# Performance work log

Hardware: AMD Instinct MI355X
Metric: run time of the kernel (lower is better)

The kernel has to match this reference:

```python
import jax, jax.numpy as jnp
import numpy as np

B, T, C = 2, 2048, 2048
NH, NKV, D = 16, 4, 128
N_REP = NH // NKV
THETA = 10000.0


def setup_inputs() -> dict:
    key = jax.random.key(0)
    ks = jax.random.split(key, 5)
    s = 0.02
    return {
        "x": jax.random.normal(ks[0], (B, T, C), dtype=jnp.float32),
        "Wq": jax.random.normal(ks[1], (C, C), dtype=jnp.float32) * s,
        "Wk": jax.random.normal(ks[2], (NKV * D, C), dtype=jnp.float32) * s,
        "Wv": jax.random.normal(ks[3], (NKV * D, C), dtype=jnp.float32) * s,
        "Wo": jax.random.normal(ks[4], (C, C), dtype=jnp.float32) * s,
    }


def _rope(t):
    # t: (B, H, T, D); rotate pairs (even, odd) by angle pos * theta_i
    inv_freq = 1.0 / (THETA ** (jnp.arange(0, D, 2, dtype=jnp.float32) / D))  # (D/2,)
    ang = jnp.arange(T, dtype=jnp.float32)[:, None] * inv_freq[None, :]       # (T, D/2)
    cos, sin = jnp.cos(ang), jnp.sin(ang)
    te, to = t[..., 0::2], t[..., 1::2]
    re = te * cos - to * sin
    ro = te * sin + to * cos
    return jnp.stack([re, ro], axis=-1).reshape(t.shape).astype(t.dtype)


def reference(x, Wq, Wk, Wv, Wo):
    # Projections (Linear: y = x @ W.T)
    q = (x @ Wq.T).reshape(B, T, NH, D).transpose(0, 2, 1, 3)    # (B,NH,T,D)
    k = (x @ Wk.T).reshape(B, T, NKV, D).transpose(0, 2, 1, 3)   # (B,NKV,T,D)
    v = (x @ Wv.T).reshape(B, T, NKV, D).transpose(0, 2, 1, 3)
    q = _rope(q)
    k = _rope(k)
    # GQA: group query heads per kv head instead of materializing repeated K/V
    qg = q.reshape(B, NKV, N_REP, T, D)                          # (B,G,R,T,D)
    scale = 1.0 / jnp.sqrt(jnp.float32(D))
    scores = jnp.einsum("bgrtd,bgsd->bgrts", qg, k) * scale      # (B,G,R,T,T)
    causal = jnp.tril(jnp.ones((T, T), dtype=bool))
    scores = jnp.where(causal, scores, jnp.finfo(scores.dtype).min)
    attn = jax.nn.softmax(scores, axis=-1)
    out = jnp.einsum("bgrts,bgsd->bgrtd", attn, v)               # (B,G,R,T,D)
    out = out.reshape(B, NH, T, D).transpose(0, 2, 1, 3).reshape(B, T, C)
    return out @ Wo.T
```

## Files before the change

kernel.cpp:

```cpp
#include <hip/hip_runtime.h>
#include <hip/hip_bf16.h>
#include <stdint.h>

#define B_   2
#define T_   2048
#define C_   2048
#define NH_  16
#define NKV_ 4
#define D_   128
#define NREP_ 4

typedef __attribute__((ext_vector_type(8))) short bf16x8;
typedef __attribute__((ext_vector_type(4))) float f32x4;

__device__ inline short f2bs(float f) {
    __hip_bfloat16 h = __float2bfloat16(f);
    return *reinterpret_cast<short*>(&h);
}
__device__ inline float bs2f(unsigned short s) {
    __hip_bfloat16 h = *reinterpret_cast<__hip_bfloat16*>(&s);
    return __bfloat162float(h);
}

__device__ inline void gl_lds16(const __hip_bfloat16* g, __hip_bfloat16* l) {
    __builtin_amdgcn_global_load_lds(
        (const __attribute__((address_space(1))) unsigned int*)g,
        (__attribute__((address_space(3))) unsigned int*)l,
        16, 0, 0);
}

__global__ void cvt_f32_bf16(const float* __restrict__ src,
                             __hip_bfloat16* __restrict__ dst, int n) {
    int i = (blockIdx.x * blockDim.x + threadIdx.x) * 4;
    if (i >= n) return;
    float4 v = *reinterpret_cast<const float4*>(src + i);
    short4 o;
    o.x = f2bs(v.x); o.y = f2bs(v.y); o.z = f2bs(v.z); o.w = f2bs(v.w);
    *reinterpret_cast<short4*>(dst + i) = o;
}

__device__ inline void storeC(float* p, float v) { *p = v; }
__device__ inline void storeC(__hip_bfloat16* p, float v) { *p = __float2bfloat16(v); }

template <typename OutT>
__global__ __launch_bounds__(256) void gemm_bt(const __hip_bfloat16* __restrict__ A,
                                               const __hip_bfloat16* __restrict__ Bm,
                                               OutT* __restrict__ Cm,
                                               int M, int N, int K) {
    __shared__ __hip_bfloat16 As[128 * 32];
    __shared__ __hip_bfloat16 Bs[128 * 32];
    const int tid  = threadIdx.x;
    const int lane = tid & 63;
    const int wv   = tid >> 6;
    const int m0 = blockIdx.y * 128, n0 = blockIdx.x * 128;
    const int wm = (wv >> 1) * 64, wn = (wv & 1) * 64;
    const int q16 = lane >> 4, r16 = lane & 15;

    f32x4 acc[4][4] = {};

    const int lrow = tid >> 2;
    const int lcol = (tid & 3) * 8;
    const __hip_bfloat16* aG = A  + (size_t)(m0 + lrow) * K + lcol;
    const __hip_bfloat16* bG = Bm + (size_t)(n0 + lrow) * K + lcol;
    __hip_bfloat16* aL = As + tid * 8;
    __hip_bfloat16* bL = Bs + tid * 8;

    for (int k0 = 0; k0 < K; k0 += 32) {
        __syncthreads();
        gl_lds16(aG + k0,          aL);
        gl_lds16(aG + 64 * K + k0, aL + 2048);
        gl_lds16(bG + k0,          bL);
        gl_lds16(bG + 64 * K + k0, bL + 2048);
        __syncthreads();
        bf16x8 af[4], bfr[4];
#pragma unroll
        for (int i = 0; i < 4; i++)
            af[i] = *reinterpret_cast<const bf16x8*>(As + (wm + i * 16 + r16) * 32 + q16 * 8);
#pragma unroll
        for (int j = 0; j < 4; j++)
            bfr[j] = *reinterpret_cast<const bf16x8*>(Bs + (wn + j * 16 + r16) * 32 + q16 * 8);
#pragma unroll
        for (int i = 0; i < 4; i++)
#pragma unroll
            for (int j = 0; j < 4; j++)
                acc[i][j] = __builtin_amdgcn_mfma_f32_16x16x32_bf16(af[i], bfr[j], acc[i][j], 0, 0, 0);
    }

#pragma unroll
    for (int i = 0; i < 4; i++)
#pragma unroll
        for (int j = 0; j < 4; j++)
#pragma unroll
            for (int r = 0; r < 4; r++) {
                int row = m0 + wm + i * 16 + q16 * 4 + r;
                int col = n0 + wn + j * 16 + r16;
                storeC(&Cm[(size_t)row * N + col], acc[i][j][r]);
            }
}

__global__ void rope_scatter(const __hip_bfloat16* __restrict__ y,
                             __hip_bfloat16* __restrict__ qo,
                             __hip_bfloat16* __restrict__ ko,
                             __hip_bfloat16* __restrict__ vT) {
    int idx = blockIdx.x * blockDim.x + threadIdx.x;
    if (idx >= (B_ * T_) * 1536) return;
    int m = idx / 1536, pc = idx % 1536;
    int b = m / T_, t = m % T_;
    int n = pc * 2;
    ushort2 uv = *reinterpret_cast<const ushort2*>(y + (size_t)m * 3072 + n);
    float e = bs2f(uv.x), od = bs2f(uv.y);

    if (n < 2560) {
        int nn = (n < 2048) ? n : (n - 2048);
        int dloc = nn & 127;
        int p = dloc >> 1;
        float inv = __expf(-(float)p * (9.210340371976184f / 64.0f));
        float ang = (float)t * inv;
        float c = cosf(ang), s = sinf(ang);
        float re = e * c - od * s;
        float ro = e * s + od * c;
        ushort2 w;
        w.x = (unsigned short)f2bs(re);
        w.y = (unsigned short)f2bs(ro);
        if (n < 2048) {
            int h = n >> 7;
            *reinterpret_cast<ushort2*>(qo + ((size_t)(b * NH_ + h) * T_ + t) * D_ + dloc) = w;
        } else {
            int h = nn >> 7;
            *reinterpret_cast<ushort2*>(ko + ((size_t)(b * NKV_ + h) * T_ + t) * D_ + dloc) = w;
        }
    } else {
        int nn = n - 2560;
        int h = nn >> 7, d = nn & 127;
        __hip_bfloat16* base = vT + (size_t)(b * NKV_ + h) * D_ * T_;
        base[(size_t)d * T_ + t]       = __float2bfloat16(e);
        base[(size_t)(d + 1) * T_ + t] = __float2bfloat16(od);
    }
}

__device__ inline bf16x8 pf_gather(const ushort4& w0, const ushort4& w1,
                                   int q16, int r16) {
    int2 a0 = *reinterpret_cast<const int2*>(&w0);
    int2 a1 = *reinterpret_cast<const int2*>(&w1);
    int srcLo = ((q16 & 1) << 5) + r16;
    int srcHi = srcLo + 16;
    int lo0x = __shfl(a0.x, srcLo), lo0y = __shfl(a0.y, srcLo);
    int lo1x = __shfl(a1.x, srcLo), lo1y = __shfl(a1.y, srcLo);
    int hi0x = __shfl(a0.x, srcHi), hi0y = __shfl(a0.y, srcHi);
    int hi1x = __shfl(a1.x, srcHi), hi1y = __shfl(a1.y, srcHi);
    bool lw = (q16 < 2);
    int4 pk;
    pk.x = lw ? lo0x : lo1x;
    pk.y = lw ? lo0y : lo1y;
    pk.z = lw ? hi0x : hi1x;
    pk.w = lw ? hi0y : hi1y;
    return *reinterpret_cast<bf16x8*>(&pk);
}

__global__ __launch_bounds__(256, 3) void attn_kernel(const __hip_bfloat16* __restrict__ Q,
                                                      const __hip_bfloat16* __restrict__ Kt,
                                                      const __hip_bfloat16* __restrict__ Vt,
                                                      __hip_bfloat16* __restrict__ Op0,
                                                      __hip_bfloat16* __restrict__ Op1,
                                                      float* __restrict__ LiP) {
    __shared__ __hip_bfloat16 Ks[2][4096];
    __shared__ __hip_bfloat16 Vs[2][4096];

    const int lane = threadIdx.x & 63, wv = threadIdx.x >> 6;
    const int bg = blockIdx.y;
    const int xr = 127 - (int)blockIdx.x;
    const int tb = xr >> 1, half = xr & 1;
    const int b = bg >> 2, g = bg & 3;
    const int h = g * 4 + wv;
    const int t0 = tb * 32;
    const int q16 = lane >> 4, r16 = lane & 15;

    const int n = tb + 1;

    const __hip_bfloat16* qh = Q + ((size_t)((b * NH_ + h) * T_) + t0) * D_;
    const __hip_bfloat16* kh = Kt + (size_t)(b * NKV_ + g) * T_ * D_;
    const __hip_bfloat16* vh = Vt + (size_t)(b * NKV_ + g) * D_ * T_;

    bf16x8 bqA[4], bqB[4];
#pragma unroll
    for (int kk = 0; kk < 4; kk++) {
        bqA[kk] = *reinterpret_cast<const bf16x8*>(qh + (size_t)r16 * D_ + kk * 32 + q16 * 8);
        bqB[kk] = *reinterpret_cast<const bf16x8*>(qh + (size_t)(16 + r16) * D_ + kk * 32 + q16 * 8);
    }

    float liA = 0.f, liB = 0.f;
    f32x4 oA[8], oB[8];
#pragma unroll
    for (int d = 0; d < 8; d++) {
        oA[d] = (f32x4){0.f, 0.f, 0.f, 0.f};
        oB[d] = (f32x4){0.f, 0.f, 0.f, 0.f};
    }

    const float SCL2 = 0.088388347648318447f * 1.4426950408889634f;
    const int tqA = t0 + r16;
    const int tqB = t0 + 16 + r16;

    const __hip_bfloat16* gK = kh + (size_t)((wv & 1) * 16 + r16) * D_ + q16 * 8;
    const __hip_bfloat16* gV = vh + (size_t)(((wv - 2) * 4) * 16 + r16) * T_ + q16 * 8;

#define STAGE(bufi, s0_)                                                        \
    do {                                                                        \
        if (wv < 2) {                                                           \
            const __hip_bfloat16* gp = gK + (size_t)(s0_) * D_;                 \
            __hip_bfloat16* lp = &Ks[bufi][(wv * 4) * 512] + lane * 8;          \
            gl_lds16(gp,      lp);                                              \
            gl_lds16(gp + 32, lp + 512);                                        \
            gl_lds16(gp + 64, lp + 1024);                                       \
            gl_lds16(gp + 96, lp + 1536);                                       \
        } else {                                                                \
            const __hip_bfloat16* gp = gV + (s0_);                              \
            __hip_bfloat16* lp = &Vs[bufi][((wv - 2) * 4) * 512] + lane * 8;    \
            gl_lds16(gp,                      lp);                              \
            gl_lds16(gp + (size_t)16 * T_,    lp + 512);                        \
            gl_lds16(gp + (size_t)32 * T_,    lp + 1024);                       \
            gl_lds16(gp + (size_t)48 * T_,    lp + 1536);                       \
        }                                                                       \
    } while (0)

    if (half < n) STAGE(0, half * 32);

    int j = 0;
    for (int it = half; it < n; it += 2, j++) {
        const int s0 = it * 32;
        const int cur = j & 1;
        __syncthreads();
        if (it + 2 < n) STAGE(cur ^ 1, (it + 2) * 32);

        f32x4 sc0A = (f32x4){0.f, 0.f, 0.f, 0.f};
        f32x4 sc1A = (f32x4){0.f, 0.f, 0.f, 0.f};
        f32x4 sc0B = (f32x4){0.f, 0.f, 0.f, 0.f};
        f32x4 sc1B = (f32x4){0.f, 0.f, 0.f, 0.f};
        {
            bf16x8 ak[4];
#pragma unroll
            for (int kk = 0; kk < 4; kk++)
                ak[kk] = *reinterpret_cast<const bf16x8*>(&Ks[cur][kk * 512] + lane * 8);
#pragma unroll
            for (int kk = 0; kk < 4; kk++) {
                sc0A = __builtin_amdgcn_mfma_f32_16x16x32_bf16(ak[kk], bqA[kk], sc0A, 0, 0, 0);
                sc0B = __builtin_amdgcn_mfma_f32_16x16x32_bf16(ak[kk], bqB[kk], sc0B, 0, 0, 0);
            }
#pragma unroll
            for (int kk = 0; kk < 4; kk++)
                ak[kk] = *reinterpret_cast<const bf16x8*>(&Ks[cur][(4 + kk) * 512] + lane * 8);
#pragma unroll
            for (int kk = 0; kk < 4; kk++) {
                sc1A = __builtin_amdgcn_mfma_f32_16x16x32_bf16(ak[kk], bqA[kk], sc1A, 0, 0, 0);
                sc1B = __builtin_amdgcn_mfma_f32_16x16x32_bf16(ak[kk], bqB[kk], sc1B, 0, 0, 0);
            }
        }

        ushort4 w0A, w1A, w0B, w1B;
        float psA = 0.f, psB = 0.f;
#pragma unroll
        for (int r = 0; r < 4; r++) {
            int s_a = s0 + q16 * 4 + r;
            float pa0 = (s_a <= tqA)      ? __builtin_amdgcn_exp2f(sc0A[r] * SCL2) : 0.f;
            float pa1 = (s_a + 16 <= tqA) ? __builtin_amdgcn_exp2f(sc1A[r] * SCL2) : 0.f;
            float pb0 = (s_a <= tqB)      ? __builtin_amdgcn_exp2f(sc0B[r] * SCL2) : 0.f;
            float pb1 = (s_a + 16 <= tqB) ? __builtin_amdgcn_exp2f(sc1B[r] * SCL2) : 0.f;
            psA += pa0 + pa1;
            psB += pb0 + pb1;
            ((unsigned short*)&w0A)[r] = (unsigned short)f2bs(pa0);
            ((unsigned short*)&w1A)[r] = (unsigned short)f2bs(pa1);
            ((unsigned short*)&w0B)[r] = (unsigned short)f2bs(pb0);
            ((unsigned short*)&w1B)[r] = (unsigned short)f2bs(pb1);
        }
        liA += psA;
        liB += psB;

        bf16x8 pfA = pf_gather(w0A, w1A, q16, r16);
        bf16x8 pfB = pf_gather(w0B, w1B, q16, r16);

#pragma unroll
        for (int d = 0; d < 8; d++) {
            bf16x8 bv = *reinterpret_cast<const bf16x8*>(&Vs[cur][d * 512] + lane * 8);
            oA[d] = __builtin_amdgcn_mfma_f32_16x16x32_bf16(pfA, bv, oA[d], 0, 0, 0);
            oB[d] = __builtin_amdgcn_mfma_f32_16x16x32_bf16(pfB, bv, oB[d], 0, 0, 0);
        }
    }

    liA += __shfl_xor(liA, 16);
    liA += __shfl_xor(liA, 32);
    liB += __shfl_xor(liB, 16);
    liB += __shfl_xor(liB, 32);

    const int tile = bg * 64 + tb;
    __hip_bfloat16* od = (half ? Op1 : Op0) + ((size_t)(tile * 4 + wv)) * 4096;
#pragma unroll
    for (int r = 0; r < 4; r++) {
        int qA = q16 * 4 + r;
#pragma unroll
        for (int d = 0; d < 8; d++) {
            od[qA * 128 + d * 16 + r16]        = __float2bfloat16(oA[d][r]);
            od[(qA + 16) * 128 + d * 16 + r16] = __float2bfloat16(oB[d][r]);
        }
    }
    float* lp = LiP + ((size_t)(tile * 2 + half)) * 128 + wv * 32;
    if (q16 == 0) lp[r16] = liA;
    if (q16 == 1) lp[16 + r16] = liB;
#undef STAGE
}

__global__ void attn_combine(const __hip_bfloat16* __restrict__ O0,
                             const __hip_bfloat16* __restrict__ O1,
                             const float* __restrict__ Li,
                             __hip_bfloat16* __restrict__ Ao) {
    int idx = blockIdx.x * blockDim.x + threadIdx.x;
    int dv   = idx & 15;
    int q    = (idx >> 4) & 31;
    int hw   = (idx >> 9) & 3;
    int tile = idx >> 11;
    int bg = tile >> 6, tb = tile & 63;
    int b = bg >> 2, g = bg & 3;

    size_t obase = ((size_t)(tile * 4 + hw)) * 4096 + q * 128 + dv * 8;
    bf16x8 v0 = *reinterpret_cast<const bf16x8*>(O0 + obase);
    bf16x8 v1 = *reinterpret_cast<const bf16x8*>(O1 + obase);
    float li = Li[(size_t)(tile * 2) * 128 + hw * 32 + q] +
               Li[(size_t)(tile * 2 + 1) * 128 + hw * 32 + q];
    float inv = 1.0f / li;

    int t = tb * 32 + q;
    int h = g * 4 + hw;
    bf16x8 ov;
#pragma unroll
    for (int j = 0; j < 8; j++) {
        float s = bs2f(((const unsigned short*)&v0)[j]) + bs2f(((const unsigned short*)&v1)[j]);
        ov[j] = f2bs(s * inv);
    }
    *reinterpret_cast<bf16x8*>(Ao + ((size_t)(b * T_ + t)) * C_ + h * D_ + dv * 8) = ov;
}

extern "C" void kernel_launch(void* const* d_in, const int* in_sizes, int n_in,
                              void* d_out, int out_size, void* d_ws, size_t ws_size,
                              hipStream_t stream) {
    const float* x  = (const float*)d_in[0];
    const float* Wq = (const float*)d_in[1];
    const float* Wk = (const float*)d_in[2];
    const float* Wv = (const float*)d_in[3];
    const float* Wo = (const float*)d_in[4];
    float* out = (float*)d_out;
    char* ws = (char*)d_ws;

    __hip_bfloat16* xb   = (__hip_bfloat16*)(ws + 0);
    __hip_bfloat16* wcat = (__hip_bfloat16*)(ws + 16777216);
    __hip_bfloat16* wob  = (__hip_bfloat16*)(ws + 29360128);
    __hip_bfloat16* yq   = (__hip_bfloat16*)(ws + 37748736);
    __hip_bfloat16* qatt = (__hip_bfloat16*)(ws + 62914560);
    __hip_bfloat16* katt = (__hip_bfloat16*)(ws + 79691776);
    __hip_bfloat16* vT   = (__hip_bfloat16*)(ws + 83886080);
    __hip_bfloat16* aout = (__hip_bfloat16*)(ws + 88080384);

    __hip_bfloat16* Op0 = (__hip_bfloat16*)(ws + 0);
    __hip_bfloat16* Op1 = (__hip_bfloat16*)(ws + 37748736);
    float*          LiP = (float*)(ws + 54525952);

    const int thr = 256;
    cvt_f32_bf16<<<(B_ * T_ * C_ / 4 + thr - 1) / thr, thr, 0, stream>>>(x, xb, B_ * T_ * C_);
    cvt_f32_bf16<<<(C_ * C_ / 4 + thr - 1) / thr, thr, 0, stream>>>(Wq, wcat, C_ * C_);
    cvt_f32_bf16<<<(512 * 2048 / 4 + thr - 1) / thr, thr, 0, stream>>>(Wk, wcat + C_ * C_, 512 * 2048);
    cvt_f32_bf16<<<(512 * 2048 / 4 + thr - 1) / thr, thr, 0, stream>>>(Wv, wcat + C_ * C_ + 512 * 2048, 512 * 2048);
    cvt_f32_bf16<<<(C_ * C_ / 4 + thr - 1) / thr, thr, 0, stream>>>(Wo, wob, C_ * C_);

    gemm_bt<__hip_bfloat16><<<dim3(24, 32), 256, 0, stream>>>(xb, wcat, yq, 4096, 3072, 2048);

    rope_scatter<<<(B_ * T_ * 1536 + thr - 1) / thr, thr, 0, stream>>>(yq, qatt, katt, vT);

    attn_kernel<<<dim3(128, 8), 256, 0, stream>>>(qatt, katt, vT, Op0, Op1, LiP);
    attn_combine<<<4096, 256, 0, stream>>>(Op0, Op1, LiP, aout);

    gemm_bt<float><<<dim3(16, 32), 256, 0, stream>>>(aout, wob, out, 4096, 2048, 2048);
}
```

Before: 348.8 us.

## Enlarge attention query tile, merge conversions, split V transpose kernel

Attention blocks now each handle 64 query rows per head as four 16-row subtiles. Each K/V tile staged in LDS is reused across twice as many queries, and fully masked subtiles skip their score MFMAs. The five f32-to-bf16 conversion launches become one kernel. The V transpose moves out of the RoPE kernel into its own kernel that writes 8-element vectors instead of scattered scalar stores. The larger tile raises register pressure (occupancy hint lowered from 3 to 2) and halves the grid, which risks worse load balance.

```diff
diff --git a/kernel.cpp b/kernel.cpp
--- a/kernel.cpp
+++ b/kernel.cpp
@@ -29,10 +29,20 @@
         16, 0, 0);
 }
 
-__global__ void cvt_f32_bf16(const float* __restrict__ src,
-                             __hip_bfloat16* __restrict__ dst, int n) {
-    int i = (blockIdx.x * blockDim.x + threadIdx.x) * 4;
-    if (i >= n) return;
+__global__ void cvt_all(const float* __restrict__ x,  const float* __restrict__ Wq,
+                        const float* __restrict__ Wk, const float* __restrict__ Wv,
+                        const float* __restrict__ Wo,
+                        __hip_bfloat16* __restrict__ xb,
+                        __hip_bfloat16* __restrict__ wcat,
+                        __hip_bfloat16* __restrict__ wob) {
+    int q = blockIdx.x * blockDim.x + threadIdx.x;
+    const float* src; __hip_bfloat16* dst; int off;
+    if (q < 2097152)      { src = x;  dst = xb;             off = q; }
+    else if (q < 3145728) { src = Wq; dst = wcat;           off = q - 2097152; }
+    else if (q < 3407872) { src = Wk; dst = wcat + 4194304; off = q - 3145728; }
+    else if (q < 3670016) { src = Wv; dst = wcat + 5242880; off = q - 3407872; }
+    else                  { src = Wo; dst = wob;            off = q - 3670016; }
+    int i = off * 4;
     float4 v = *reinterpret_cast<const float4*>(src + i);
     short4 o;
     o.x = f2bs(v.x); o.y = f2bs(v.y); o.z = f2bs(v.z); o.w = f2bs(v.w);
@@ -98,44 +108,58 @@
             }
 }
 
-__global__ void rope_scatter(const __hip_bfloat16* __restrict__ y,
-                             __hip_bfloat16* __restrict__ qo,
-                             __hip_bfloat16* __restrict__ ko,
-                             __hip_bfloat16* __restrict__ vT) {
+__global__ void rope_qk(const __hip_bfloat16* __restrict__ y,
+                        __hip_bfloat16* __restrict__ qo,
+                        __hip_bfloat16* __restrict__ ko) {
     int idx = blockIdx.x * blockDim.x + threadIdx.x;
-    if (idx >= (B_ * T_) * 1536) return;
-    int m = idx / 1536, pc = idx % 1536;
+    if (idx >= (B_ * T_) * 1280) return;
+    int m = idx / 1280, pc = idx % 1280;
     int b = m / T_, t = m % T_;
     int n = pc * 2;
     ushort2 uv = *reinterpret_cast<const ushort2*>(y + (size_t)m * 3072 + n);
     float e = bs2f(uv.x), od = bs2f(uv.y);
 
-    if (n < 2560) {
-        int nn = (n < 2048) ? n : (n - 2048);
-        int dloc = nn & 127;
-        int p = dloc >> 1;
-        float inv = __expf(-(float)p * (9.210340371976184f / 64.0f));
-        float ang = (float)t * inv;
-        float c = cosf(ang), s = sinf(ang);
-        float re = e * c - od * s;
-        float ro = e * s + od * c;
-        ushort2 w;
-        w.x = (unsigned short)f2bs(re);
-        w.y = (unsigned short)f2bs(ro);
-        if (n < 2048) {
-            int h = n >> 7;
-            *reinterpret_cast<ushort2*>(qo + ((size_t)(b * NH_ + h) * T_ + t) * D_ + dloc) = w;
-        } else {
-            int h = nn >> 7;
-            *reinterpret_cast<ushort2*>(ko + ((size_t)(b * NKV_ + h) * T_ + t) * D_ + dloc) = w;
-        }
+    int nn = (n < 2048) ? n : (n - 2048);
+    int dloc = nn & 127;
+    int p = dloc >> 1;
+    float inv = __expf(-(float)p * (9.210340371976184f / 64.0f));
+    float ang = (float)t * inv;
+    float c = cosf(ang), s = sinf(ang);
+    float re = e * c - od * s;
+    float ro = e * s + od * c;
+    ushort2 w;
+    w.x = (unsigned short)f2bs(re);
+    w.y = (unsigned short)f2bs(ro);
+    if (n < 2048) {
+        int h = n >> 7;
+        *reinterpret_cast<ushort2*>(qo + ((size_t)(b * NH_ + h) * T_ + t) * D_ + dloc) = w;
     } else {
-        int nn = n - 2560;
-        int h = nn >> 7, d = nn & 127;
-        __hip_bfloat16* base = vT + (size_t)(b * NKV_ + h) * D_ * T_;
-        base[(size_t)d * T_ + t]       = __float2bfloat16(e);
-        base[(size_t)(d + 1) * T_ + t] = __float2bfloat16(od);
-    }
+        int h = nn >> 7;
+        *reinterpret_cast<ushort2*>(ko + ((size_t)(b * NKV_ + h) * T_ + t) * D_ + dloc) = w;
+    }
+}
+
+__global__ void v_transpose(const __hip_bfloat16* __restrict__ y,
+                            __hip_bfloat16* __restrict__ vT) {
+    int idx = blockIdx.x * blockDim.x + threadIdx.x;
+    int tc = idx & 255;
+    int d  = (idx >> 8) & 127;
+    int gg = (idx >> 15) & 3;
+    int b  = idx >> 17;
+    int t0 = tc * 8;
+    const __hip_bfloat16* src = y + (size_t)(b * T_ + t0) * 3072 + 2560 + gg * 128 + d;
+    ushort4 w0, w1;
+    ((unsigned short*)&w0)[0] = *(const unsigned short*)(src);
+    ((unsigned short*)&w0)[1] = *(const unsigned short*)(src + 3072);
+    ((unsigned short*)&w0)[2] = *(const unsigned short*)(src + 2 * 3072);
+    ((unsigned short*)&w0)[3] = *(const unsigned short*)(src + 3 * 3072);
+    ((unsigned short*)&w1)[0] = *(const unsigned short*)(src + 4 * 3072);
+    ((unsigned short*)&w1)[1] = *(const unsigned short*)(src + 5 * 3072);
+    ((unsigned short*)&w1)[2] = *(const unsigned short*)(src + 6 * 3072);
+    ((unsigned short*)&w1)[3] = *(const unsigned short*)(src + 7 * 3072);
+    __hip_bfloat16* dst = vT + ((size_t)(b * NKV_ + gg) * D_ + d) * T_ + t0;
+    *reinterpret_cast<ushort4*>(dst)     = w0;
+    *reinterpret_cast<ushort4*>(dst + 4) = w1;
 }
 
 __device__ inline bf16x8 pf_gather(const ushort4& w0, const ushort4& w1,
@@ -157,7 +181,7 @@
     return *reinterpret_cast<bf16x8*>(&pk);
 }
 
-__global__ __launch_bounds__(256, 3) void attn_kernel(const __hip_bfloat16* __restrict__ Q,
+__global__ __launch_bounds__(256, 2) void attn_kernel(const __hip_bfloat16* __restrict__ Q,
                                                       const __hip_bfloat16* __restrict__ Kt,
                                                       const __hip_bfloat16* __restrict__ Vt,
                                                       __hip_bfloat16* __restrict__ Op0,
@@ -168,37 +192,35 @@
 
     const int lane = threadIdx.x & 63, wv = threadIdx.x >> 6;
     const int bg = blockIdx.y;
-    const int xr = 127 - (int)blockIdx.x;
+    const int xr = 63 - (int)blockIdx.x;
     const int tb = xr >> 1, half = xr & 1;
     const int b = bg >> 2, g = bg & 3;
     const int h = g * 4 + wv;
-    const int t0 = tb * 32;
+    const int t0 = tb * 64;
     const int q16 = lane >> 4, r16 = lane & 15;
 
-    const int n = tb + 1;
+    const int n = 2 * (tb + 1);
 
     const __hip_bfloat16* qh = Q + ((size_t)((b * NH_ + h) * T_) + t0) * D_;
     const __hip_bfloat16* kh = Kt + (size_t)(b * NKV_ + g) * T_ * D_;
     const __hip_bfloat16* vh = Vt + (size_t)(b * NKV_ + g) * D_ * T_;
 
-    bf16x8 bqA[4], bqB[4];
-#pragma unroll
-    for (int kk = 0; kk < 4; kk++) {
-        bqA[kk] = *reinterpret_cast<const bf16x8*>(qh + (size_t)r16 * D_ + kk * 32 + q16 * 8);
-        bqB[kk] = *reinterpret_cast<const bf16x8*>(qh + (size_t)(16 + r16) * D_ + kk * 32 + q16 * 8);
-    }
-
-    float liA = 0.f, liB = 0.f;
-    f32x4 oA[8], oB[8];
-#pragma unroll
-    for (int d = 0; d < 8; d++) {
-        oA[d] = (f32x4){0.f, 0.f, 0.f, 0.f};
-        oB[d] = (f32x4){0.f, 0.f, 0.f, 0.f};
-    }
+    bf16x8 bq[4][4];
+#pragma unroll
+    for (int tile = 0; tile < 4; tile++)
+#pragma unroll
+        for (int kk = 0; kk < 4; kk++)
+            bq[tile][kk] = *reinterpret_cast<const bf16x8*>(
+                qh + (size_t)(tile * 16 + r16) * D_ + kk * 32 + q16 * 8);
+
+    float li[4] = {0.f, 0.f, 0.f, 0.f};
+    f32x4 acc[4][8];
+#pragma unroll
+    for (int tile = 0; tile < 4; tile++)
+#pragma unroll
+        for (int d = 0; d < 8; d++) acc[tile][d] = (f32x4){0.f, 0.f, 0.f, 0.f};
 
     const float SCL2 = 0.088388347648318447f * 1.4426950408889634f;
-    const int tqA = t0 + r16;
-    const int tqB = t0 + 16 + r16;
 
     const __hip_bfloat16* gK = kh + (size_t)((wv & 1) * 16 + r16) * D_ + q16 * 8;
     const __hip_bfloat16* gV = vh + (size_t)(((wv - 2) * 4) * 16 + r16) * T_ + q16 * 8;
@@ -231,79 +253,74 @@
         __syncthreads();
         if (it + 2 < n) STAGE(cur ^ 1, (it + 2) * 32);
 
-        f32x4 sc0A = (f32x4){0.f, 0.f, 0.f, 0.f};
-        f32x4 sc1A = (f32x4){0.f, 0.f, 0.f, 0.f};
-        f32x4 sc0B = (f32x4){0.f, 0.f, 0.f, 0.f};
-        f32x4 sc1B = (f32x4){0.f, 0.f, 0.f, 0.f};
-        {
-            bf16x8 ak[4];
-#pragma unroll
-            for (int kk = 0; kk < 4; kk++)
-                ak[kk] = *reinterpret_cast<const bf16x8*>(&Ks[cur][kk * 512] + lane * 8);
-#pragma unroll
-            for (int kk = 0; kk < 4; kk++) {
-                sc0A = __builtin_amdgcn_mfma_f32_16x16x32_bf16(ak[kk], bqA[kk], sc0A, 0, 0, 0);
-                sc0B = __builtin_amdgcn_mfma_f32_16x16x32_bf16(ak[kk], bqB[kk], sc0B, 0, 0, 0);
-            }
-#pragma unroll
-            for (int kk = 0; kk < 4; kk++)
-                ak[kk] = *reinterpret_cast<const bf16x8*>(&Ks[cur][(4 + kk) * 512] + lane * 8);
-#pragma unroll
-            for (int kk = 0; kk < 4; kk++) {
-                sc1A = __builtin_amdgcn_mfma_f32_16x16x32_bf16(ak[kk], bqA[kk], sc1A, 0, 0, 0);
-                sc1B = __builtin_amdgcn_mfma_f32_16x16x32_bf16(ak[kk], bqB[kk], sc1B, 0, 0, 0);
+        bf16x8 akl[4], akh[4];
+#pragma unroll
+        for (int kk = 0; kk < 4; kk++) {
+            akl[kk] = *reinterpret_cast<const bf16x8*>(&Ks[cur][kk * 512] + lane * 8);
+            akh[kk] = *reinterpret_cast<const bf16x8*>(&Ks[cur][(4 + kk) * 512] + lane * 8);
+        }
+
+        bf16x8 pf[4];
+#pragma unroll
+        for (int tile = 0; tile < 4; tile++) {
+            if (s0 <= t0 + tile * 16 + 15) {
+                f32x4 sc0 = (f32x4){0.f, 0.f, 0.f, 0.f};
+                f32x4 sc1 = (f32x4){0.f, 0.f, 0.f, 0.f};
+#pragma unroll
+                for (int kk = 0; kk < 4; kk++) {
+                    sc0 = __builtin_amdgcn_mfma_f32_16x16x32_bf16(akl[kk], bq[tile][kk], sc0, 0, 0, 0);
+                    sc1 = __builtin_amdgcn_mfma_f32_16x16x32_bf16(akh[kk], bq[tile][kk], sc1, 0, 0, 0);
+                }
+                const int tq = t0 + tile * 16 + r16;
+                ushort4 w0, w1;
+                float ps = 0.f;
+#pragma unroll
+                for (int r = 0; r < 4; r++) {
+                    int s_a = s0 + q16 * 4 + r;
+                    float p0 = (s_a <= tq)      ? __builtin_amdgcn_exp2f(sc0[r] * SCL2) : 0.f;
+                    float p1 = (s_a + 16 <= tq) ? __builtin_amdgcn_exp2f(sc1[r] * SCL2) : 0.f;
+                    ps += p0 + p1;
+                    ((unsigned short*)&w0)[r] = (unsigned short)f2bs(p0);
+                    ((unsigned short*)&w1)[r] = (unsigned short)f2bs(p1);
+                }
+                li[tile] += ps;
+                pf[tile] = pf_gather(w0, w1, q16, r16);
+            } else {
+                int4 z = (int4){0, 0, 0, 0};
+                pf[tile] = *reinterpret_cast<bf16x8*>(&z);
             }
         }
 
-        ushort4 w0A, w1A, w0B, w1B;
-        float psA = 0.f, psB = 0.f;
-#pragma unroll
-        for (int r = 0; r < 4; r++) {
-            int s_a = s0 + q16 * 4 + r;
-            float pa0 = (s_a <= tqA)      ? __builtin_amdgcn_exp2f(sc0A[r] * SCL2) : 0.f;
-            float pa1 = (s_a + 16 <= tqA) ? __builtin_amdgcn_exp2f(sc1A[r] * SCL2) : 0.f;
-            float pb0 = (s_a <= tqB)      ? __builtin_amdgcn_exp2f(sc0B[r] * SCL2) : 0.f;
-            float pb1 = (s_a + 16 <= tqB) ? __builtin_amdgcn_exp2f(sc1B[r] * SCL2) : 0.f;
-            psA += pa0 + pa1;
-            psB += pb0 + pb1;
-            ((unsigned short*)&w0A)[r] = (unsigned short)f2bs(pa0);
-            ((unsigned short*)&w1A)[r] = (unsigned short)f2bs(pa1);
-            ((unsigned short*)&w0B)[r] = (unsigned short)f2bs(pb0);
-            ((unsigned short*)&w1B)[r] = (unsigned short)f2bs(pb1);
-        }
-        liA += psA;
-        liB += psB;
-
-        bf16x8 pfA = pf_gather(w0A, w1A, q16, r16);
-        bf16x8 pfB = pf_gather(w0B, w1B, q16, r16);
-
 #pragma unroll
         for (int d = 0; d < 8; d++) {
             bf16x8 bv = *reinterpret_cast<const bf16x8*>(&Vs[cur][d * 512] + lane * 8);
-            oA[d] = __builtin_amdgcn_mfma_f32_16x16x32_bf16(pfA, bv, oA[d], 0, 0, 0);
-            oB[d] = __builtin_amdgcn_mfma_f32_16x16x32_bf16(pfB, bv, oB[d], 0, 0, 0);
+#pragma unroll
+            for (int tile = 0; tile < 4; tile++)
+                acc[tile][d] = __builtin_amdgcn_mfma_f32_16x16x32_bf16(pf[tile], bv, acc[tile][d], 0, 0, 0);
         }
     }
 
-    liA += __shfl_xor(liA, 16);
-    liA += __shfl_xor(liA, 32);
-    liB += __shfl_xor(liB, 16);
-    liB += __shfl_xor(liB, 32);
-
-    const int tile = bg * 64 + tb;
-    __hip_bfloat16* od = (half ? Op1 : Op0) + ((size_t)(tile * 4 + wv)) * 4096;
-#pragma unroll
-    for (int r = 0; r < 4; r++) {
-        int qA = q16 * 4 + r;
-#pragma unroll
-        for (int d = 0; d < 8; d++) {
-            od[qA * 128 + d * 16 + r16]        = __float2bfloat16(oA[d][r]);
-            od[(qA + 16) * 128 + d * 16 + r16] = __float2bfloat16(oB[d][r]);
+#pragma unroll
+    for (int tile = 0; tile < 4; tile++) {
+        li[tile] += __shfl_xor(li[tile], 16);
+        li[tile] += __shfl_xor(li[tile], 32);
+    }
+
+    const int tileG = bg * 32 + tb;
+    __hip_bfloat16* od = (half ? Op1 : Op0) + ((size_t)(tileG * 4 + wv)) * 8192;
+#pragma unroll
+    for (int tile = 0; tile < 4; tile++)
+#pragma unroll
+        for (int r = 0; r < 4; r++) {
+            int qA = tile * 16 + q16 * 4 + r;
+#pragma unroll
+            for (int d = 0; d < 8; d++)
+                od[qA * 128 + d * 16 + r16] = __float2bfloat16(acc[tile][d][r]);
         }
-    }
-    float* lp = LiP + ((size_t)(tile * 2 + half)) * 128 + wv * 32;
-    if (q16 == 0) lp[r16] = liA;
-    if (q16 == 1) lp[16 + r16] = liB;
+
+    float lv = (q16 == 0) ? li[0] : (q16 == 1) ? li[1] : (q16 == 2) ? li[2] : li[3];
+    float* lp = LiP + ((size_t)((tileG * 2 + half) * 4 + wv)) * 64;
+    lp[q16 * 16 + r16] = lv;
 #undef STAGE
 }
 
@@ -312,21 +329,21 @@
                              const float* __restrict__ Li,
                              __hip_bfloat16* __restrict__ Ao) {
     int idx = blockIdx.x * blockDim.x + threadIdx.x;
-    int dv   = idx & 15;
-    int q    = (idx >> 4) & 31;
-    int hw   = (idx >> 9) & 3;
-    int tile = idx >> 11;
-    int bg = tile >> 6, tb = tile & 63;
+    int dv    = idx & 15;
+    int q     = (idx >> 4) & 63;
+    int hw    = (idx >> 10) & 3;
+    int tileG = idx >> 12;
+    int bg = tileG >> 5, tb = tileG & 31;
     int b = bg >> 2, g = bg & 3;
 
-    size_t obase = ((size_t)(tile * 4 + hw)) * 4096 + q * 128 + dv * 8;
+    size_t obase = ((size_t)(tileG * 4 + hw)) * 8192 + q * 128 + dv * 8;
     bf16x8 v0 = *reinterpret_cast<const bf16x8*>(O0 + obase);
     bf16x8 v1 = *reinterpret_cast<const bf16x8*>(O1 + obase);
-    float li = Li[(size_t)(tile * 2) * 128 + hw * 32 + q] +
-               Li[(size_t)(tile * 2 + 1) * 128 + hw * 32 + q];
+    float li = Li[((size_t)((tileG * 2) * 4 + hw)) * 64 + q] +
+               Li[((size_t)((tileG * 2 + 1) * 4 + hw)) * 64 + q];
     float inv = 1.0f / li;
 
-    int t = tb * 32 + q;
+    int t = tb * 64 + q;
     int h = g * 4 + hw;
     bf16x8 ov;
 #pragma unroll
@@ -362,17 +379,14 @@
     float*          LiP = (float*)(ws + 54525952);
 
     const int thr = 256;
-    cvt_f32_bf16<<<(B_ * T_ * C_ / 4 + thr - 1) / thr, thr, 0, stream>>>(x, xb, B_ * T_ * C_);
-    cvt_f32_bf16<<<(C_ * C_ / 4 + thr - 1) / thr, thr, 0, stream>>>(Wq, wcat, C_ * C_);
-    cvt_f32_bf16<<<(512 * 2048 / 4 + thr - 1) / thr, thr, 0, stream>>>(Wk, wcat + C_ * C_, 512 * 2048);
-    cvt_f32_bf16<<<(512 * 2048 / 4 + thr - 1) / thr, thr, 0, stream>>>(Wv, wcat + C_ * C_ + 512 * 2048, 512 * 2048);
-    cvt_f32_bf16<<<(C_ * C_ / 4 + thr - 1) / thr, thr, 0, stream>>>(Wo, wob, C_ * C_);
+    cvt_all<<<18432, thr, 0, stream>>>(x, Wq, Wk, Wv, Wo, xb, wcat, wob);
 
     gemm_bt<__hip_bfloat16><<<dim3(24, 32), 256, 0, stream>>>(xb, wcat, yq, 4096, 3072, 2048);
 
-    rope_scatter<<<(B_ * T_ * 1536 + thr - 1) / thr, thr, 0, stream>>>(yq, qatt, katt, vT);
-
-    attn_kernel<<<dim3(128, 8), 256, 0, stream>>>(qatt, katt, vT, Op0, Op1, LiP);
+    rope_qk<<<(B_ * T_ * 1280 + thr - 1) / thr, thr, 0, stream>>>(yq, qatt, katt);
+    v_transpose<<<1024, thr, 0, stream>>>(yq, vT);
+
+    attn_kernel<<<dim3(64, 8), 256, 0, stream>>>(qatt, katt, vT, Op0, Op1, LiP);
     attn_combine<<<4096, 256, 0, stream>>>(Op0, Op1, LiP, aout);
 
     gemm_bt<float><<<dim3(16, 32), 256, 0, stream>>>(aout, wob, out, 4096, 2048, 2048);
```

After: 372.4 us. 1.07x slower.

## Fuse conversions, split V transpose, pair causal tiles per attention block

Applied to the files above, without the earlier changes.

The five fp32-to-bf16 conversion launches become one kernel that picks its source by index range. The V part of rope_scatter moves into its own transpose kernel, where each thread writes eight consecutive timesteps as vector stores instead of scattered 2-byte writes. The attention grid is halved, and each block now processes a short causal tile and its mirrored long tile one after the other, to balance work across blocks. In exchange the V transpose now does strided 2-byte reads, and each attention block runs twice as long.

```diff
diff --git a/kernel.cpp b/kernel.cpp
--- a/kernel.cpp
+++ b/kernel.cpp
@@ -29,10 +29,20 @@
         16, 0, 0);
 }
 
-__global__ void cvt_f32_bf16(const float* __restrict__ src,
-                             __hip_bfloat16* __restrict__ dst, int n) {
-    int i = (blockIdx.x * blockDim.x + threadIdx.x) * 4;
-    if (i >= n) return;
+__global__ void cvt_all(const float* __restrict__ x,  const float* __restrict__ Wq,
+                        const float* __restrict__ Wk, const float* __restrict__ Wv,
+                        const float* __restrict__ Wo,
+                        __hip_bfloat16* __restrict__ xb,
+                        __hip_bfloat16* __restrict__ wcat,
+                        __hip_bfloat16* __restrict__ wob) {
+    int q = blockIdx.x * blockDim.x + threadIdx.x;
+    const float* src; __hip_bfloat16* dst; int off;
+    if (q < 2097152)      { src = x;  dst = xb;             off = q; }
+    else if (q < 3145728) { src = Wq; dst = wcat;           off = q - 2097152; }
+    else if (q < 3407872) { src = Wk; dst = wcat + 4194304; off = q - 3145728; }
+    else if (q < 3670016) { src = Wv; dst = wcat + 5242880; off = q - 3407872; }
+    else                  { src = Wo; dst = wob;            off = q - 3670016; }
+    int i = off * 4;
     float4 v = *reinterpret_cast<const float4*>(src + i);
     short4 o;
     o.x = f2bs(v.x); o.y = f2bs(v.y); o.z = f2bs(v.z); o.w = f2bs(v.w);
@@ -98,44 +108,58 @@
             }
 }
 
-__global__ void rope_scatter(const __hip_bfloat16* __restrict__ y,
-                             __hip_bfloat16* __restrict__ qo,
-                             __hip_bfloat16* __restrict__ ko,
-                             __hip_bfloat16* __restrict__ vT) {
+__global__ void rope_qk(const __hip_bfloat16* __restrict__ y,
+                        __hip_bfloat16* __restrict__ qo,
+                        __hip_bfloat16* __restrict__ ko) {
     int idx = blockIdx.x * blockDim.x + threadIdx.x;
-    if (idx >= (B_ * T_) * 1536) return;
-    int m = idx / 1536, pc = idx % 1536;
+    if (idx >= (B_ * T_) * 1280) return;
+    int m = idx / 1280, pc = idx % 1280;
     int b = m / T_, t = m % T_;
     int n = pc * 2;
     ushort2 uv = *reinterpret_cast<const ushort2*>(y + (size_t)m * 3072 + n);
     float e = bs2f(uv.x), od = bs2f(uv.y);
 
-    if (n < 2560) {
-        int nn = (n < 2048) ? n : (n - 2048);
-        int dloc = nn & 127;
-        int p = dloc >> 1;
-        float inv = __expf(-(float)p * (9.210340371976184f / 64.0f));
-        float ang = (float)t * inv;
-        float c = cosf(ang), s = sinf(ang);
-        float re = e * c - od * s;
-        float ro = e * s + od * c;
-        ushort2 w;
-        w.x = (unsigned short)f2bs(re);
-        w.y = (unsigned short)f2bs(ro);
-        if (n < 2048) {
-            int h = n >> 7;
-            *reinterpret_cast<ushort2*>(qo + ((size_t)(b * NH_ + h) * T_ + t) * D_ + dloc) = w;
-        } else {
-            int h = nn >> 7;
-            *reinterpret_cast<ushort2*>(ko + ((size_t)(b * NKV_ + h) * T_ + t) * D_ + dloc) = w;
-        }
+    int nn = (n < 2048) ? n : (n - 2048);
+    int dloc = nn & 127;
+    int p = dloc >> 1;
+    float inv = __expf(-(float)p * (9.210340371976184f / 64.0f));
+    float ang = (float)t * inv;
+    float c = cosf(ang), s = sinf(ang);
+    float re = e * c - od * s;
+    float ro = e * s + od * c;
+    ushort2 w;
+    w.x = (unsigned short)f2bs(re);
+    w.y = (unsigned short)f2bs(ro);
+    if (n < 2048) {
+        int h = n >> 7;
+        *reinterpret_cast<ushort2*>(qo + ((size_t)(b * NH_ + h) * T_ + t) * D_ + dloc) = w;
     } else {
-        int nn = n - 2560;
-        int h = nn >> 7, d = nn & 127;
-        __hip_bfloat16* base = vT + (size_t)(b * NKV_ + h) * D_ * T_;
-        base[(size_t)d * T_ + t]       = __float2bfloat16(e);
-        base[(size_t)(d + 1) * T_ + t] = __float2bfloat16(od);
+        int h = nn >> 7;
+        *reinterpret_cast<ushort2*>(ko + ((size_t)(b * NKV_ + h) * T_ + t) * D_ + dloc) = w;
     }
+}
+
+__global__ void v_transpose(const __hip_bfloat16* __restrict__ y,
+                            __hip_bfloat16* __restrict__ vT) {
+    int idx = blockIdx.x * blockDim.x + threadIdx.x;
+    int tc = idx & 255;
+    int d  = (idx >> 8) & 127;
+    int gg = (idx >> 15) & 3;
+    int b  = idx >> 17;
+    int t0 = tc * 8;
+    const __hip_bfloat16* src = y + (size_t)(b * T_ + t0) * 3072 + 2560 + gg * 128 + d;
+    ushort4 w0, w1;
+    ((unsigned short*)&w0)[0] = *(const unsigned short*)(src);
+    ((unsigned short*)&w0)[1] = *(const unsigned short*)(src + 3072);
+    ((unsigned short*)&w0)[2] = *(const unsigned short*)(src + 2 * 3072);
+    ((unsigned short*)&w0)[3] = *(const unsigned short*)(src + 3 * 3072);
+    ((unsigned short*)&w1)[0] = *(const unsigned short*)(src + 4 * 3072);
+    ((unsigned short*)&w1)[1] = *(const unsigned short*)(src + 5 * 3072);
+    ((unsigned short*)&w1)[2] = *(const unsigned short*)(src + 6 * 3072);
+    ((unsigned short*)&w1)[3] = *(const unsigned short*)(src + 7 * 3072);
+    __hip_bfloat16* dst = vT + ((size_t)(b * NKV_ + gg) * D_ + d) * T_ + t0;
+    *reinterpret_cast<ushort4*>(dst)     = w0;
+    *reinterpret_cast<ushort4*>(dst + 4) = w1;
 }
 
 __device__ inline bf16x8 pf_gather(const ushort4& w0, const ushort4& w1,
@@ -168,40 +192,17 @@
 
     const int lane = threadIdx.x & 63, wv = threadIdx.x >> 6;
     const int bg = blockIdx.y;
-    const int xr = 127 - (int)blockIdx.x;
-    const int tb = xr >> 1, half = xr & 1;
+    const int bx = (int)blockIdx.x;
     const int b = bg >> 2, g = bg & 3;
     const int h = g * 4 + wv;
-    const int t0 = tb * 32;
     const int q16 = lane >> 4, r16 = lane & 15;
 
-    const int n = tb + 1;
-
-    const __hip_bfloat16* qh = Q + ((size_t)((b * NH_ + h) * T_) + t0) * D_;
     const __hip_bfloat16* kh = Kt + (size_t)(b * NKV_ + g) * T_ * D_;
     const __hip_bfloat16* vh = Vt + (size_t)(b * NKV_ + g) * D_ * T_;
-
-    bf16x8 bqA[4], bqB[4];
-#pragma unroll
-    for (int kk = 0; kk < 4; kk++) {
-        bqA[kk] = *reinterpret_cast<const bf16x8*>(qh + (size_t)r16 * D_ + kk * 32 + q16 * 8);
-        bqB[kk] = *reinterpret_cast<const bf16x8*>(qh + (size_t)(16 + r16) * D_ + kk * 32 + q16 * 8);
-    }
-
-    float liA = 0.f, liB = 0.f;
-    f32x4 oA[8], oB[8];
-#pragma unroll
-    for (int d = 0; d < 8; d++) {
-        oA[d] = (f32x4){0.f, 0.f, 0.f, 0.f};
-        oB[d] = (f32x4){0.f, 0.f, 0.f, 0.f};
-    }
-
-    const float SCL2 = 0.088388347648318447f * 1.4426950408889634f;
-    const int tqA = t0 + r16;
-    const int tqB = t0 + 16 + r16;
-
     const __hip_bfloat16* gK = kh + (size_t)((wv & 1) * 16 + r16) * D_ + q16 * 8;
     const __hip_bfloat16* gV = vh + (size_t)(((wv - 2) * 4) * 16 + r16) * T_ + q16 * 8;
+
+    const float SCL2 = 0.088388347648318447f * 1.4426950408889634f;
 
 #define STAGE(bufi, s0_)                                                        \
     do {                                                                        \
@@ -222,88 +223,116 @@
         }                                                                       \
     } while (0)
 
-    if (half < n) STAGE(0, half * 32);
-
-    int j = 0;
-    for (int it = half; it < n; it += 2, j++) {
-        const int s0 = it * 32;
-        const int cur = j & 1;
-        __syncthreads();
-        if (it + 2 < n) STAGE(cur ^ 1, (it + 2) * 32);
-
-        f32x4 sc0A = (f32x4){0.f, 0.f, 0.f, 0.f};
-        f32x4 sc1A = (f32x4){0.f, 0.f, 0.f, 0.f};
-        f32x4 sc0B = (f32x4){0.f, 0.f, 0.f, 0.f};
-        f32x4 sc1B = (f32x4){0.f, 0.f, 0.f, 0.f};
-        {
-            bf16x8 ak[4];
-#pragma unroll
-            for (int kk = 0; kk < 4; kk++)
-                ak[kk] = *reinterpret_cast<const bf16x8*>(&Ks[cur][kk * 512] + lane * 8);
-#pragma unroll
-            for (int kk = 0; kk < 4; kk++) {
-                sc0A = __builtin_amdgcn_mfma_f32_16x16x32_bf16(ak[kk], bqA[kk], sc0A, 0, 0, 0);
-                sc0B = __builtin_amdgcn_mfma_f32_16x16x32_bf16(ak[kk], bqB[kk], sc0B, 0, 0, 0);
+    for (int ph = 0; ph < 2; ph++) {
+        const int xr = ph ? (127 - bx) : bx;
+        const int tb = xr >> 1, half = xr & 1;
+        const int t0 = tb * 32;
+        const int n = tb + 1;
+
+        const __hip_bfloat16* qh = Q + ((size_t)((b * NH_ + h) * T_) + t0) * D_;
+        bf16x8 bqA[4], bqB[4];
+#pragma unroll
+        for (int kk = 0; kk < 4; kk++) {
+            bqA[kk] = *reinterpret_cast<const bf16x8*>(qh + (size_t)r16 * D_ + kk * 32 + q16 * 8);
+            bqB[kk] = *reinterpret_cast<const bf16x8*>(qh + (size_t)(16 + r16) * D_ + kk * 32 + q16 * 8);
+        }
+
+        float liA = 0.f, liB = 0.f;
+        f32x4 oA[8], oB[8];
+#pragma unroll
+        for (int d = 0; d < 8; d++) {
+            oA[d] = (f32x4){0.f, 0.f, 0.f, 0.f};
+            oB[d] = (f32x4){0.f, 0.f, 0.f, 0.f};
+        }
+
+        const int tqA = t0 + r16;
+        const int tqB = t0 + 16 + r16;
+
+        if (half < n) STAGE(0, half * 32);
+
+        int j = 0;
+        for (int it = half; it < n; it += 2, j++) {
+            const int s0 = it * 32;
+            const int cur = j & 1;
+            __syncthreads();
+            if (it + 2 < n) STAGE(cur ^ 1, (it + 2) * 32);
+
+            f32x4 sc0A = (f32x4){0.f, 0.f, 0.f, 0.f};
+            f32x4 sc1A = (f32x4){0.f, 0.f, 0.f, 0.f};
+            f32x4 sc0B = (f32x4){0.f, 0.f, 0.f, 0.f};
+            f32x4 sc1B = (f32x4){0.f, 0.f, 0.f, 0.f};
+            {
+                bf16x8 ak[4];
+#pragma unroll
+                for (int kk = 0; kk < 4; kk++)
+                    ak[kk] = *reinterpret_cast<const bf16x8*>(&Ks[cur][kk * 512] + lane * 8);
+#pragma unroll
+                for (int kk = 0; kk < 4; kk++) {
+                    sc0A = __builtin_amdgcn_mfma_f32_16x16x32_bf16(ak[kk], bqA[kk], sc0A, 0, 0, 0);
+                    sc0B = __builtin_amdgcn_mfma_f32_16x16x32_bf16(ak[kk], bqB[kk], sc0B, 0, 0, 0);
+                }
+#pragma unroll
+                for (int kk = 0; kk < 4; kk++)
+                    ak[kk] = *reinterpret_cast<const bf16x8*>(&Ks[cur][(4 + kk) * 512] + lane * 8);
+#pragma unroll
+                for (int kk = 0; kk < 4; kk++) {
+                    sc1A = __builtin_amdgcn_mfma_f32_16x16x32_bf16(ak[kk], bqA[kk], sc1A, 0, 0, 0);
+                    sc1B = __builtin_amdgcn_mfma_f32_16x16x32_bf16(ak[kk], bqB[kk], sc1B, 0, 0, 0);
+                }
             }
-#pragma unroll
-            for (int kk = 0; kk < 4; kk++)
-                ak[kk] = *reinterpret_cast<const bf16x8*>(&Ks[cur][(4 + kk) * 512] + lane * 8);
-#pragma unroll
-            for (int kk = 0; kk < 4; kk++) {
-                sc1A = __builtin_amdgcn_mfma_f32_16x16x32_bf16(ak[kk], bqA[kk], sc1A, 0, 0, 0);
-                sc1B = __builtin_amdgcn_mfma_f32_16x16x32_bf16(ak[kk], bqB[kk], sc1B, 0, 0, 0);
+
+            ushort4 w0A, w1A, w0B, w1B;
+            float psA = 0.f, psB = 0.f;
+#pragma unroll
+            for (int r = 0; r < 4; r++) {
+                int s_a = s0 + q16 * 4 + r;
+                float pa0 = (s_a <= tqA)      ? __builtin_amdgcn_exp2f(sc0A[r] * SCL2) : 0.f;
+                float pa1 = (s_a + 16 <= tqA) ? __builtin_amdgcn_exp2f(sc1A[r] * SCL2) : 0.f;
+                float pb0 = (s_a <= tqB)      ? __builtin_amdgcn_exp2f(sc0B[r] * SCL2) : 0.f;
+                float pb1 = (s_a + 16 <= tqB) ? __builtin_amdgcn_exp2f(sc1B[r] * SCL2) : 0.f;
+                psA += pa0 + pa1;
+                psB += pb0 + pb1;
+                ((unsigned short*)&w0A)[r] = (unsigned short)f2bs(pa0);
+                ((unsigned short*)&w1A)[r] = (unsigned short)f2bs(pa1);
+                ((unsigned short*)&w0B)[r] = (unsigned short)f2bs(pb0);
+                ((unsigned short*)&w1B)[r] = (unsigned short)f2bs(pb1);
+            }
+            liA += psA;
+            liB += psB;
+
+            bf16x8 pfA = pf_gather(w0A, w1A, q16, r16);
+            bf16x8 pfB = pf_gather(w0B, w1B, q16, r16);
+
+#pragma unroll
+            for (int d = 0; d < 8; d++) {
+                bf16x8 bv = *reinterpret_cast<const bf16x8*>(&Vs[cur][d * 512] + lane * 8);
+                oA[d] = __builtin_amdgcn_mfma_f32_16x16x32_bf16(pfA, bv, oA[d], 0, 0, 0);
+                oB[d] = __builtin_amdgcn_mfma_f32_16x16x32_bf16(pfB, bv, oB[d], 0, 0, 0);
             }
         }
 
-        ushort4 w0A, w1A, w0B, w1B;
-        float psA = 0.f, psB = 0.f;
+        liA += __shfl_xor(liA, 16);
+        liA += __shfl_xor(liA, 32);
+        liB += __shfl_xor(liB, 16);
+        liB += __shfl_xor(liB, 32);
+
+        const int tile = bg * 64 + tb;
+        __hip_bfloat16* od = (half ? Op1 : Op0) + ((size_t)(tile * 4 + wv)) * 4096;
 #pragma unroll
         for (int r = 0; r < 4; r++) {
-            int s_a = s0 + q16 * 4 + r;
-            float pa0 = (s_a <= tqA)      ? __builtin_amdgcn_exp2f(sc0A[r] * SCL2) : 0.f;
-            float pa1 = (s_a + 16 <= tqA) ? __builtin_amdgcn_exp2f(sc1A[r] * SCL2) : 0.f;
-            float pb0 = (s_a <= tqB)      ? __builtin_amdgcn_exp2f(sc0B[r] * SCL2) : 0.f;
-            float pb1 = (s_a + 16 <= tqB) ? __builtin_amdgcn_exp2f(sc1B[r] * SCL2) : 0.f;
-            psA += pa0 + pa1;
-            psB += pb0 + pb1;
-            ((unsigned short*)&w0A)[r] = (unsigned short)f2bs(pa0);
-            ((unsigned short*)&w1A)[r] = (unsigned short)f2bs(pa1);
-            ((unsigned short*)&w0B)[r] = (unsigned short)f2bs(pb0);
-            ((unsigned short*)&w1B)[r] = (unsigned short)f2bs(pb1);
+            int qA = q16 * 4 + r;
+#pragma unroll
+            for (int d = 0; d < 8; d++) {
+                od[qA * 128 + d * 16 + r16]        = __float2bfloat16(oA[d][r]);
+                od[(qA + 16) * 128 + d * 16 + r16] = __float2bfloat16(oB[d][r]);
+            }
         }
-        liA += psA;
-        liB += psB;
-
-        bf16x8 pfA = pf_gather(w0A, w1A, q16, r16);
-        bf16x8 pfB = pf_gather(w0B, w1B, q16, r16);
-
-#pragma unroll
-        for (int d = 0; d < 8; d++) {
-            bf16x8 bv = *reinterpret_cast<const bf16x8*>(&Vs[cur][d * 512] + lane * 8);
-            oA[d] = __builtin_amdgcn_mfma_f32_16x16x32_bf16(pfA, bv, oA[d], 0, 0, 0);
-            oB[d] = __builtin_amdgcn_mfma_f32_16x16x32_bf16(pfB, bv, oB[d], 0, 0, 0);
-        }
+        float* lp = LiP + ((size_t)(tile * 2 + half)) * 128 + wv * 32;
+        if (q16 == 0) lp[r16] = liA;
+        if (q16 == 1) lp[16 + r16] = liB;
+
+        __syncthreads();
     }
-
-    liA += __shfl_xor(liA, 16);
-    liA += __shfl_xor(liA, 32);
-    liB += __shfl_xor(liB, 16);
-    liB += __shfl_xor(liB, 32);
-
-    const int tile = bg * 64 + tb;
-    __hip_bfloat16* od = (half ? Op1 : Op0) + ((size_t)(tile * 4 + wv)) * 4096;
-#pragma unroll
-    for (int r = 0; r < 4; r++) {
-        int qA = q16 * 4 + r;
-#pragma unroll
-        for (int d = 0; d < 8; d++) {
-            od[qA * 128 + d * 16 + r16]        = __float2bfloat16(oA[d][r]);
-            od[(qA + 16) * 128 + d * 16 + r16] = __float2bfloat16(oB[d][r]);
-        }
-    }
-    float* lp = LiP + ((size_t)(tile * 2 + half)) * 128 + wv * 32;
-    if (q16 == 0) lp[r16] = liA;
-    if (q16 == 1) lp[16 + r16] = liB;
 #undef STAGE
 }
 
@@ -362,17 +391,14 @@
     float*          LiP = (float*)(ws + 54525952);
 
     const int thr = 256;
-    cvt_f32_bf16<<<(B_ * T_ * C_ / 4 + thr - 1) / thr, thr, 0, stream>>>(x, xb, B_ * T_ * C_);
-    cvt_f32_bf16<<<(C_ * C_ / 4 + thr - 1) / thr, thr, 0, stream>>>(Wq, wcat, C_ * C_);
-    cvt_f32_bf16<<<(512 * 2048 / 4 + thr - 1) / thr, thr, 0, stream>>>(Wk, wcat + C_ * C_, 512 * 2048);
-    cvt_f32_bf16<<<(512 * 2048 / 4 + thr - 1) / thr, thr, 0, stream>>>(Wv, wcat + C_ * C_ + 512 * 2048, 512 * 2048);
-    cvt_f32_bf16<<<(C_ * C_ / 4 + thr - 1) / thr, thr, 0, stream>>>(Wo, wob, C_ * C_);
+    cvt_all<<<18432, thr, 0, stream>>>(x, Wq, Wk, Wv, Wo, xb, wcat, wob);
 
     gemm_bt<__hip_bfloat16><<<dim3(24, 32), 256, 0, stream>>>(xb, wcat, yq, 4096, 3072, 2048);
 
-    rope_scatter<<<(B_ * T_ * 1536 + thr - 1) / thr, thr, 0, stream>>>(yq, qatt, katt, vT);
-
-    attn_kernel<<<dim3(128, 8), 256, 0, stream>>>(qatt, katt, vT, Op0, Op1, LiP);
+    rope_qk<<<(B_ * T_ * 1280 + thr - 1) / thr, thr, 0, stream>>>(yq, qatt, katt);
+    v_transpose<<<1024, thr, 0, stream>>>(yq, vT);
+
+    attn_kernel<<<dim3(64, 8), 256, 0, stream>>>(qatt, katt, vT, Op0, Op1, LiP);
     attn_combine<<<4096, 256, 0, stream>>>(Op0, Op1, LiP, aout);
 
     gemm_bt<float><<<dim3(16, 32), 256, 0, stream>>>(aout, wob, out, 4096, 2048, 2048);
```

Result: no change. 343.0 us (-1.7%).
